# Optimization experiments

Hardware: AMD Instinct MI355X
Metric: run time of the kernel (lower is better)

Reference implementation:

```python
import jax, jax.numpy as jnp
import numpy as np

N, D = 1024, 512
BS, N_TEXT, N_VIDEO = 64, 16, 16
BETA = 1.0
N_ITERS = 50


def setup_inputs() -> dict:
    key = jax.random.key(0)
    k1, k2 = jax.random.split(key)
    return {
        "t_prob": jax.random.normal(k1, (N, D), dtype=jnp.float32),
        "v_prob": jax.random.normal(k2, (N, D), dtype=jnp.float32),
        "n": N,
        "bs": BS,
        "n_text": N_TEXT,
        "n_video": N_VIDEO,
    }


def _l2norm(x):
    # matches F.normalize(x, p=2, dim=1) (eps irrelevant for randn inputs)
    return x / jnp.linalg.norm(x, axis=1, keepdims=True)


def reference(t_prob, v_prob, n, bs, n_text, n_video):
    dt = t_prob.dtype
    x = _l2norm(t_prob)
    y = _l2norm(v_prob)
    C = 1.0 - x @ y.T                      # [n, n] cosine distance
    A = jnp.exp(-C / BETA)

    sigma0 = jnp.ones((n, 1), dtype=dt) / n
    T0 = jnp.ones((n, n), dtype=dt)

    def step(carry, _):
        T, sigma = carry
        Q = A * T                          # [n, n]
        delta = 1.0 / (n * (Q @ sigma))    # [n, 1]
        sigma_new = 1.0 / (n * (Q.T @ delta))  # [n, 1]
        # diag(delta) @ Q @ diag(sigma) == row/col rescale
        T_new = delta * Q * sigma_new.T
        return (T_new, sigma_new), None

    (T, _), _ = jax.lax.scan(step, (T0, sigma0), None, length=N_ITERS)

    distance_matrix = C.T @ T              # [n, n]
    distance_matrix = distance_matrix.reshape(bs, n_text, bs, n_video).mean(axis=(1, 3))
    dis_loss = jnp.trace(distance_matrix)
    return distance_matrix, dis_loss
```

## Files before the change

kernel.cpp:

```cpp
#include <hip/hip_runtime.h>
#include <math.h>


#define NWG 32
#define TPB 256
#define NIT 50
#define NREP 4

typedef unsigned long long ull;

constexpr int CL_OFF   = 0;
constexpr int CVEC_OFF = 1024 * 1024;
constexpr int CNT_OFF  = CVEC_OFF + 3 * NREP * 1024;

__global__ __launch_bounds__(256) void k_gemm(const float* __restrict__ X,
                                              const float* __restrict__ Y,
                                              float* __restrict__ ws) {
    __shared__ float As[32][68];
    __shared__ float Bs[32][68];
    __shared__ float nX[64], nY[64];
    float* Cl = ws + CL_OFF;

    int tid = threadIdx.x;
    int tx = tid & 15, ty = tid >> 4;
    int bx = blockIdx.x, by = blockIdx.y;
    int lr0 = tid >> 3;
    int kq  = (tid & 7) * 4;

    float acc[4][4] = {};
    float sx0 = 0.f, sx1 = 0.f, sy0 = 0.f, sy1 = 0.f;
    for (int k0 = 0; k0 < 512; k0 += 32) {
        float4 xa = *(const float4*)(X + (size_t)(by * 64 + lr0) * 512 + k0 + kq);
        float4 xb = *(const float4*)(X + (size_t)(by * 64 + lr0 + 32) * 512 + k0 + kq);
        float4 ya = *(const float4*)(Y + (size_t)(bx * 64 + lr0) * 512 + k0 + kq);
        float4 yb = *(const float4*)(Y + (size_t)(bx * 64 + lr0 + 32) * 512 + k0 + kq);
        sx0 += xa.x * xa.x + xa.y * xa.y + xa.z * xa.z + xa.w * xa.w;
        sx1 += xb.x * xb.x + xb.y * xb.y + xb.z * xb.z + xb.w * xb.w;
        sy0 += ya.x * ya.x + ya.y * ya.y + ya.z * ya.z + ya.w * ya.w;
        sy1 += yb.x * yb.x + yb.y * yb.y + yb.z * yb.z + yb.w * yb.w;
        As[kq + 0][lr0] = xa.x; As[kq + 1][lr0] = xa.y;
        As[kq + 2][lr0] = xa.z; As[kq + 3][lr0] = xa.w;
        As[kq + 0][lr0 + 32] = xb.x; As[kq + 1][lr0 + 32] = xb.y;
        As[kq + 2][lr0 + 32] = xb.z; As[kq + 3][lr0 + 32] = xb.w;
        Bs[kq + 0][lr0] = ya.x; Bs[kq + 1][lr0] = ya.y;
        Bs[kq + 2][lr0] = ya.z; Bs[kq + 3][lr0] = ya.w;
        Bs[kq + 0][lr0 + 32] = yb.x; Bs[kq + 1][lr0 + 32] = yb.y;
        Bs[kq + 2][lr0 + 32] = yb.z; Bs[kq + 3][lr0 + 32] = yb.w;
        __syncthreads();
#pragma unroll
        for (int kk = 0; kk < 32; ++kk) {
            float4 a4 = *(const float4*)&As[kk][4 * ty];
            float4 b4 = *(const float4*)&Bs[kk][4 * tx];
            float av[4] = {a4.x, a4.y, a4.z, a4.w};
            float bv[4] = {b4.x, b4.y, b4.z, b4.w};
#pragma unroll
            for (int r = 0; r < 4; ++r)
#pragma unroll
                for (int q = 0; q < 4; ++q) acc[r][q] += av[r] * bv[q];
        }
        __syncthreads();
    }
#pragma unroll
    for (int m = 1; m < 8; m <<= 1) {
        sx0 += __shfl_xor(sx0, m, 64);
        sx1 += __shfl_xor(sx1, m, 64);
        sy0 += __shfl_xor(sy0, m, 64);
        sy1 += __shfl_xor(sy1, m, 64);
    }
    if ((tid & 7) == 0) {
        nX[lr0] = sx0; nX[lr0 + 32] = sx1;
        nY[lr0] = sy0; nY[lr0 + 32] = sy1;
    }
    __syncthreads();

    int i0 = by * 64 + 4 * ty, j0 = bx * 64 + 4 * tx;
    float vy[4];
#pragma unroll
    for (int q = 0; q < 4; ++q) vy[q] = 1.0f / sqrtf(nY[4 * tx + q]);
#pragma unroll
    for (int r = 0; r < 4; ++r) {
        float vx = 1.0f / sqrtf(nX[4 * ty + r]);
        float4 o;
        o.x = acc[r][0] * vx * vy[0] - 1.0f;
        o.y = acc[r][1] * vx * vy[1] - 1.0f;
        o.z = acc[r][2] * vx * vy[2] - 1.0f;
        o.w = acc[r][3] * vx * vy[3] - 1.0f;
        *(float4*)(Cl + (size_t)(i0 + r) * 1024 + j0) = o;
    }
}

__global__ __launch_bounds__(256, 1) void k_ipot(float* __restrict__ ws,
                                                 float* __restrict__ out) {
    __shared__ float sL[1024];
    __shared__ float aL[32];
    __shared__ float buf[4 * 1024];
    __shared__ float twv[4];

    const int g = blockIdx.x, tid = threadIdx.x;
    const int rs = tid >> 6, lane = tid & 63;
    float* Cl   = ws + CL_OFF;
    float* cvec = ws + CVEC_OFF;
    unsigned* grp = (unsigned*)(ws + CNT_OFF);

    float C[8][16], E[8][16];
#pragma unroll
    for (int i = 0; i < 8; ++i) {
        const float* src = Cl + (size_t)(g * 32 + rs * 8 + i) * 1024 + lane * 16;
#pragma unroll
        for (int q = 0; q < 4; ++q) {
            float4 c = *(const float4*)(src + 4 * q);
            C[i][4 * q + 0] = c.x; C[i][4 * q + 1] = c.y;
            C[i][4 * q + 2] = c.z; C[i][4 * q + 3] = c.w;
        }
    }
#pragma unroll
    for (int i = 0; i < 8; ++i)
#pragma unroll
        for (int u = 0; u < 16; ++u) E[i][u] = __expf(C[i][u]);

    float bv[4] = {1.0f, 1.0f, 1.0f, 1.0f};

    for (int t = 0; t < NIT; ++t) {
        if (t == 0) {
            *(float4*)&sL[4 * tid] =
                make_float4(1/1024.f, 1/1024.f, 1/1024.f, 1/1024.f);
        } else {
            if (tid == 0) {
                unsigned tgt = (unsigned)t * 8u;
                long gd = 0;
                while (__hip_atomic_load(&grp[0], __ATOMIC_RELAXED, __HIP_MEMORY_SCOPE_AGENT) < tgt ||
                       __hip_atomic_load(&grp[1], __ATOMIC_RELAXED, __HIP_MEMORY_SCOPE_AGENT) < tgt ||
                       __hip_atomic_load(&grp[2], __ATOMIC_RELAXED, __HIP_MEMORY_SCOPE_AGENT) < tgt ||
                       __hip_atomic_load(&grp[3], __ATOMIC_RELAXED, __HIP_MEMORY_SCOPE_AGENT) < tgt) {
                    __builtin_amdgcn_s_sleep(1);
                    if (++gd > 2000000) break;
                }
            }
            __syncthreads();
            const ull* rb = (const ull*)(cvec + ((t + 2) % 3) * (NREP * 1024)) + 2 * tid;
            ull u00 = __hip_atomic_load(rb + 0 * 512,     __ATOMIC_RELAXED, __HIP_MEMORY_SCOPE_AGENT);
            ull u01 = __hip_atomic_load(rb + 0 * 512 + 1, __ATOMIC_RELAXED, __HIP_MEMORY_SCOPE_AGENT);
            ull u10 = __hip_atomic_load(rb + 1 * 512,     __ATOMIC_RELAXED, __HIP_MEMORY_SCOPE_AGENT);
            ull u11 = __hip_atomic_load(rb + 1 * 512 + 1, __ATOMIC_RELAXED, __HIP_MEMORY_SCOPE_AGENT);
            ull u20 = __hip_atomic_load(rb + 2 * 512,     __ATOMIC_RELAXED, __HIP_MEMORY_SCOPE_AGENT);
            ull u21 = __hip_atomic_load(rb + 2 * 512 + 1, __ATOMIC_RELAXED, __HIP_MEMORY_SCOPE_AGENT);
            ull u30 = __hip_atomic_load(rb + 3 * 512,     __ATOMIC_RELAXED, __HIP_MEMORY_SCOPE_AGENT);
            ull u31 = __hip_atomic_load(rb + 3 * 512 + 1, __ATOMIC_RELAXED, __HIP_MEMORY_SCOPE_AGENT);
            if (t >= 2 && tid < 64) {
                ull* zb = (ull*)(cvec + ((t + 1) % 3) * (NREP * 1024)) + g * 64 + tid;
                __hip_atomic_store(zb, 0ull, __ATOMIC_RELAXED, __HIP_MEMORY_SCOPE_AGENT);
            }
            float c0 = __uint_as_float((unsigned)u00) + __uint_as_float((unsigned)u10) +
                       __uint_as_float((unsigned)u20) + __uint_as_float((unsigned)u30);
            float c1 = __uint_as_float((unsigned)(u00 >> 32)) + __uint_as_float((unsigned)(u10 >> 32)) +
                       __uint_as_float((unsigned)(u20 >> 32)) + __uint_as_float((unsigned)(u30 >> 32));
            float c2 = __uint_as_float((unsigned)u01) + __uint_as_float((unsigned)u11) +
                       __uint_as_float((unsigned)u21) + __uint_as_float((unsigned)u31);
            float c3 = __uint_as_float((unsigned)(u01 >> 32)) + __uint_as_float((unsigned)(u11 >> 32)) +
                       __uint_as_float((unsigned)(u21 >> 32)) + __uint_as_float((unsigned)(u31 >> 32));
            float b0 = 1.0f / c0, b1 = 1.0f / c1, b2 = 1.0f / c2, b3 = 1.0f / c3;
            float4 sn;
            sn.x = b0 * b0 / bv[0] * (1.0f / 1024.0f); bv[0] = b0;
            sn.y = b1 * b1 / bv[1] * (1.0f / 1024.0f); bv[1] = b1;
            sn.z = b2 * b2 / bv[2] * (1.0f / 1024.0f); bv[2] = b2;
            sn.w = b3 * b3 / bv[3] * (1.0f / 1024.0f); bv[3] = b3;
            *(float4*)&sL[4 * tid] = sn;
        }
        __syncthreads();

        float sv[16];
#pragma unroll
        for (int q = 0; q < 4; ++q) {
            float4 s4 = *(const float4*)&sL[lane * 16 + 4 * q];
            sv[4 * q + 0] = s4.x; sv[4 * q + 1] = s4.y;
            sv[4 * q + 2] = s4.z; sv[4 * q + 3] = s4.w;
        }
        float rp[8];
#pragma unroll
        for (int i = 0; i < 8; ++i) {
            float a = 0.0f;
#pragma unroll
            for (int u = 0; u < 16; ++u) a += E[i][u] * sv[u];
            rp[i] = a;
        }
#pragma unroll
        for (int m = 1; m < 64; m <<= 1)
#pragma unroll
            for (int i = 0; i < 8; ++i) rp[i] += __shfl_xor(rp[i], m, 64);
        if (lane == 0) {
#pragma unroll
            for (int i = 0; i < 8; ++i)
                aL[rs * 8 + i] = 1.0f / (1024.0f * rp[i]);
        }
        __syncthreads();

        float av[8];
#pragma unroll
        for (int i = 0; i < 8; ++i) av[i] = aL[rs * 8 + i];
        float cp[16];
#pragma unroll
        for (int u = 0; u < 16; ++u) {
            float a = 0.0f;
#pragma unroll
            for (int i = 0; i < 8; ++i) a += E[i][u] * av[i];
            cp[u] = a;
        }
#pragma unroll
        for (int q = 0; q < 4; ++q)
            *(float4*)&buf[rs * 1024 + lane * 16 + 4 * q] =
                make_float4(cp[4*q], cp[4*q+1], cp[4*q+2], cp[4*q+3]);
        __syncthreads();

        float4 t0 = *(const float4*)&buf[0 * 1024 + 4 * tid];
        float4 t1 = *(const float4*)&buf[1 * 1024 + 4 * tid];
        float4 t2 = *(const float4*)&buf[2 * 1024 + 4 * tid];
        float4 t3 = *(const float4*)&buf[3 * 1024 + 4 * tid];
        float* wb = cvec + (t % 3) * (NREP * 1024) + (g & 3) * 1024 + 4 * tid;
        atomicAdd(wb + 0, t0.x + t1.x + t2.x + t3.x);
        atomicAdd(wb + 1, t0.y + t1.y + t2.y + t3.y);
        atomicAdd(wb + 2, t0.z + t1.z + t2.z + t3.z);
        atomicAdd(wb + 3, t0.w + t1.w + t2.w + t3.w);
        __syncthreads();
        if (tid == 0)
            __hip_atomic_fetch_add(&grp[g >> 3], 1u, __ATOMIC_RELAXED,
                                   __HIP_MEMORY_SCOPE_AGENT);

        if (t < NIT - 1) {
            const float kf = (float)(t + 2);
#pragma unroll
            for (int i = 0; i < 8; ++i)
#pragma unroll
                for (int u = 0; u < 16; ++u) E[i][u] = __expf(kf * C[i][u]);
        }
    }

    if (tid == 0) {
        unsigned tgt = (unsigned)NIT * 8u;
        long gd = 0;
        while (__hip_atomic_load(&grp[0], __ATOMIC_RELAXED, __HIP_MEMORY_SCOPE_AGENT) < tgt ||
               __hip_atomic_load(&grp[1], __ATOMIC_RELAXED, __HIP_MEMORY_SCOPE_AGENT) < tgt ||
               __hip_atomic_load(&grp[2], __ATOMIC_RELAXED, __HIP_MEMORY_SCOPE_AGENT) < tgt ||
               __hip_atomic_load(&grp[3], __ATOMIC_RELAXED, __HIP_MEMORY_SCOPE_AGENT) < tgt) {
            __builtin_amdgcn_s_sleep(1);
            if (++gd > 2000000) break;
        }
    }
    __syncthreads();
    {
        const ull* rb = (const ull*)(cvec + ((NIT - 1) % 3) * (NREP * 1024)) + 2 * tid;
        ull u00 = __hip_atomic_load(rb + 0 * 512,     __ATOMIC_RELAXED, __HIP_MEMORY_SCOPE_AGENT);
        ull u01 = __hip_atomic_load(rb + 0 * 512 + 1, __ATOMIC_RELAXED, __HIP_MEMORY_SCOPE_AGENT);
        ull u10 = __hip_atomic_load(rb + 1 * 512,     __ATOMIC_RELAXED, __HIP_MEMORY_SCOPE_AGENT);
        ull u11 = __hip_atomic_load(rb + 1 * 512 + 1, __ATOMIC_RELAXED, __HIP_MEMORY_SCOPE_AGENT);
        ull u20 = __hip_atomic_load(rb + 2 * 512,     __ATOMIC_RELAXED, __HIP_MEMORY_SCOPE_AGENT);
        ull u21 = __hip_atomic_load(rb + 2 * 512 + 1, __ATOMIC_RELAXED, __HIP_MEMORY_SCOPE_AGENT);
        ull u30 = __hip_atomic_load(rb + 3 * 512,     __ATOMIC_RELAXED, __HIP_MEMORY_SCOPE_AGENT);
        ull u31 = __hip_atomic_load(rb + 3 * 512 + 1, __ATOMIC_RELAXED, __HIP_MEMORY_SCOPE_AGENT);
        float4 bb;
        bb.x = 1.0f / (__uint_as_float((unsigned)u00) + __uint_as_float((unsigned)u10) +
                       __uint_as_float((unsigned)u20) + __uint_as_float((unsigned)u30));
        bb.y = 1.0f / (__uint_as_float((unsigned)(u00 >> 32)) + __uint_as_float((unsigned)(u10 >> 32)) +
                       __uint_as_float((unsigned)(u20 >> 32)) + __uint_as_float((unsigned)(u30 >> 32)));
        bb.z = 1.0f / (__uint_as_float((unsigned)u01) + __uint_as_float((unsigned)u11) +
                       __uint_as_float((unsigned)u21) + __uint_as_float((unsigned)u31));
        bb.w = 1.0f / (__uint_as_float((unsigned)(u01 >> 32)) + __uint_as_float((unsigned)(u11 >> 32)) +
                       __uint_as_float((unsigned)(u21 >> 32)) + __uint_as_float((unsigned)(u31 >> 32)));
        *(float4*)&sL[4 * tid] = bb;
    }
    __syncthreads();

    float* Ps = buf;
    float* Rs = buf + 2048;
    float bl[16];
#pragma unroll
    for (int q = 0; q < 4; ++q) {
        float4 b4 = *(const float4*)&sL[lane * 16 + 4 * q];
        bl[4 * q + 0] = b4.x; bl[4 * q + 1] = b4.y;
        bl[4 * q + 2] = b4.z; bl[4 * q + 3] = b4.w;
    }
#pragma unroll
    for (int i = 0; i < 8; ++i) {
        float p = 0.0f, r = 0.0f;
#pragma unroll
        for (int u = 0; u < 16; ++u) {
            p += C[i][u];
            r += E[i][u] * bl[u];
        }
        Ps[(rs * 8 + i) * 64 + lane] = -p;
        Rs[(rs * 8 + i) * 64 + lane] = aL[rs * 8 + i] * r;
    }
    __syncthreads();

    float Rk[32];
#pragma unroll
    for (int k = 0; k < 32; ++k) Rk[k] = Rs[k * 64 + lane];
    const float sc = 1.0f / (256.0f * 1024.0f);
    float tsum = 0.0f;
#pragma unroll
    for (int q = 0; q < 16; ++q) {
        int o = tid + 256 * q;
        int A = o >> 6;
        float acc = 0.0f;
#pragma unroll
        for (int k = 0; k < 32; ++k) acc += Ps[k * 64 + A] * Rk[k];
        float val = acc * sc;
        atomicAdd(out + o, val);
        if (A == lane) tsum += val;
    }
#pragma unroll
    for (int m = 1; m < 64; m <<= 1) tsum += __shfl_xor(tsum, m, 64);
    if (lane == 0) twv[rs] = tsum;
    __syncthreads();
    if (tid == 0) atomicAdd(out + 4096, twv[0] + twv[1] + twv[2] + twv[3]);
}

extern "C" void kernel_launch(void* const* d_in, const int* in_sizes, int n_in,
                              void* d_out, int out_size, void* d_ws, size_t ws_size,
                              hipStream_t stream) {
    const float* X = (const float*)d_in[0];
    const float* Y = (const float*)d_in[1];
    float* out = (float*)d_out;
    float* ws  = (float*)d_ws;

    (void)hipMemsetAsync((char*)d_ws + (size_t)CVEC_OFF * 4, 0,
                         (3 * NREP * 1024 + 16) * 4, stream);
    (void)hipMemsetAsync(d_out, 0, (size_t)out_size * 4, stream);

    k_gemm<<<dim3(16, 16), 256, 0, stream>>>(X, Y, ws);
    k_ipot<<<NWG, TPB, 0, stream>>>(ws, out);
}
```

Measured before the change: 331.3 us.

## Widen IPOT workgroups to 1024 threads with two rows per wavefront

Raises the iterative Sinkhorn-style kernel from 256 to 1024 threads per workgroup, so each of the 16 wavefronts holds 2 rows of the cost and kernel matrices instead of 8. The per-thread register footprint shrinks and the column-sum stage becomes a 16-way shared-memory reduction with one scalar atomic per thread. The intent is to put more wavefronts on each CU and hide the latency of the per-iteration matrix-vector products and the cross-workgroup barrier. In exchange, each __syncthreads spans 16 waves, the shared buffer grows fourfold, and the final tail loop is redistributed across the wider block.

```diff
diff --git a/kernel.cpp b/kernel.cpp
--- a/kernel.cpp
+++ b/kernel.cpp
@@ -3,7 +3,7 @@
 
 
 #define NWG 32
-#define TPB 256
+#define TPB 1024
 #define NIT 50
 #define NREP 4
 
@@ -89,12 +89,12 @@
     }
 }
 
-__global__ __launch_bounds__(256, 1) void k_ipot(float* __restrict__ ws,
-                                                 float* __restrict__ out) {
+__global__ __launch_bounds__(1024, 4) void k_ipot(float* __restrict__ ws,
+                                                  float* __restrict__ out) {
     __shared__ float sL[1024];
     __shared__ float aL[32];
-    __shared__ float buf[4 * 1024];
-    __shared__ float twv[4];
+    __shared__ float buf[16 * 1024];
+    __shared__ float twv[16];
 
     const int g = blockIdx.x, tid = threadIdx.x;
     const int rs = tid >> 6, lane = tid & 63;
@@ -102,10 +102,10 @@
     float* cvec = ws + CVEC_OFF;
     unsigned* grp = (unsigned*)(ws + CNT_OFF);
 
-    float C[8][16], E[8][16];
-#pragma unroll
-    for (int i = 0; i < 8; ++i) {
-        const float* src = Cl + (size_t)(g * 32 + rs * 8 + i) * 1024 + lane * 16;
+    float C[2][16], E[2][16];
+#pragma unroll
+    for (int i = 0; i < 2; ++i) {
+        const float* src = Cl + (size_t)(g * 32 + rs * 2 + i) * 1024 + lane * 16;
 #pragma unroll
         for (int q = 0; q < 4; ++q) {
             float4 c = *(const float4*)(src + 4 * q);
@@ -114,16 +114,15 @@
         }
     }
 #pragma unroll
-    for (int i = 0; i < 8; ++i)
+    for (int i = 0; i < 2; ++i)
 #pragma unroll
         for (int u = 0; u < 16; ++u) E[i][u] = __expf(C[i][u]);
 
-    float bv[4] = {1.0f, 1.0f, 1.0f, 1.0f};
+    float bv = 1.0f;
 
     for (int t = 0; t < NIT; ++t) {
         if (t == 0) {
-            *(float4*)&sL[4 * tid] =
-                make_float4(1/1024.f, 1/1024.f, 1/1024.f, 1/1024.f);
+            sL[tid] = 1.0f / 1024.0f;
         } else {
             if (tid == 0) {
                 unsigned tgt = (unsigned)t * 8u;
@@ -137,34 +136,19 @@
                 }
             }
             __syncthreads();
-            const ull* rb = (const ull*)(cvec + ((t + 2) % 3) * (NREP * 1024)) + 2 * tid;
-            ull u00 = __hip_atomic_load(rb + 0 * 512,     __ATOMIC_RELAXED, __HIP_MEMORY_SCOPE_AGENT);
-            ull u01 = __hip_atomic_load(rb + 0 * 512 + 1, __ATOMIC_RELAXED, __HIP_MEMORY_SCOPE_AGENT);
-            ull u10 = __hip_atomic_load(rb + 1 * 512,     __ATOMIC_RELAXED, __HIP_MEMORY_SCOPE_AGENT);
-            ull u11 = __hip_atomic_load(rb + 1 * 512 + 1, __ATOMIC_RELAXED, __HIP_MEMORY_SCOPE_AGENT);
-            ull u20 = __hip_atomic_load(rb + 2 * 512,     __ATOMIC_RELAXED, __HIP_MEMORY_SCOPE_AGENT);
-            ull u21 = __hip_atomic_load(rb + 2 * 512 + 1, __ATOMIC_RELAXED, __HIP_MEMORY_SCOPE_AGENT);
-            ull u30 = __hip_atomic_load(rb + 3 * 512,     __ATOMIC_RELAXED, __HIP_MEMORY_SCOPE_AGENT);
-            ull u31 = __hip_atomic_load(rb + 3 * 512 + 1, __ATOMIC_RELAXED, __HIP_MEMORY_SCOPE_AGENT);
+            const float* rb = cvec + ((t + 2) % 3) * (NREP * 1024) + tid;
+            float r0 = __hip_atomic_load(rb + 0 * 1024, __ATOMIC_RELAXED, __HIP_MEMORY_SCOPE_AGENT);
+            float r1 = __hip_atomic_load(rb + 1 * 1024, __ATOMIC_RELAXED, __HIP_MEMORY_SCOPE_AGENT);
+            float r2 = __hip_atomic_load(rb + 2 * 1024, __ATOMIC_RELAXED, __HIP_MEMORY_SCOPE_AGENT);
+            float r3 = __hip_atomic_load(rb + 3 * 1024, __ATOMIC_RELAXED, __HIP_MEMORY_SCOPE_AGENT);
             if (t >= 2 && tid < 64) {
                 ull* zb = (ull*)(cvec + ((t + 1) % 3) * (NREP * 1024)) + g * 64 + tid;
                 __hip_atomic_store(zb, 0ull, __ATOMIC_RELAXED, __HIP_MEMORY_SCOPE_AGENT);
             }
-            float c0 = __uint_as_float((unsigned)u00) + __uint_as_float((unsigned)u10) +
-                       __uint_as_float((unsigned)u20) + __uint_as_float((unsigned)u30);
-            float c1 = __uint_as_float((unsigned)(u00 >> 32)) + __uint_as_float((unsigned)(u10 >> 32)) +
-                       __uint_as_float((unsigned)(u20 >> 32)) + __uint_as_float((unsigned)(u30 >> 32));
-            float c2 = __uint_as_float((unsigned)u01) + __uint_as_float((unsigned)u11) +
-                       __uint_as_float((unsigned)u21) + __uint_as_float((unsigned)u31);
-            float c3 = __uint_as_float((unsigned)(u01 >> 32)) + __uint_as_float((unsigned)(u11 >> 32)) +
-                       __uint_as_float((unsigned)(u21 >> 32)) + __uint_as_float((unsigned)(u31 >> 32));
-            float b0 = 1.0f / c0, b1 = 1.0f / c1, b2 = 1.0f / c2, b3 = 1.0f / c3;
-            float4 sn;
-            sn.x = b0 * b0 / bv[0] * (1.0f / 1024.0f); bv[0] = b0;
-            sn.y = b1 * b1 / bv[1] * (1.0f / 1024.0f); bv[1] = b1;
-            sn.z = b2 * b2 / bv[2] * (1.0f / 1024.0f); bv[2] = b2;
-            sn.w = b3 * b3 / bv[3] * (1.0f / 1024.0f); bv[3] = b3;
-            *(float4*)&sL[4 * tid] = sn;
+            float c = r0 + r1 + r2 + r3;
+            float b = 1.0f / c;
+            sL[tid] = b * b / bv * (1.0f / 1024.0f);
+            bv = b;
         }
         __syncthreads();
 
@@ -175,51 +159,42 @@
             sv[4 * q + 0] = s4.x; sv[4 * q + 1] = s4.y;
             sv[4 * q + 2] = s4.z; sv[4 * q + 3] = s4.w;
         }
-        float rp[8];
-#pragma unroll
-        for (int i = 0; i < 8; ++i) {
+        float rp[2];
+#pragma unroll
+        for (int i = 0; i < 2; ++i) {
             float a = 0.0f;
 #pragma unroll
             for (int u = 0; u < 16; ++u) a += E[i][u] * sv[u];
             rp[i] = a;
         }
 #pragma unroll
-        for (int m = 1; m < 64; m <<= 1)
-#pragma unroll
-            for (int i = 0; i < 8; ++i) rp[i] += __shfl_xor(rp[i], m, 64);
+        for (int m = 1; m < 64; m <<= 1) {
+            rp[0] += __shfl_xor(rp[0], m, 64);
+            rp[1] += __shfl_xor(rp[1], m, 64);
+        }
         if (lane == 0) {
-#pragma unroll
-            for (int i = 0; i < 8; ++i)
-                aL[rs * 8 + i] = 1.0f / (1024.0f * rp[i]);
-        }
-        __syncthreads();
-
-        float av[8];
-#pragma unroll
-        for (int i = 0; i < 8; ++i) av[i] = aL[rs * 8 + i];
-        float cp[16];
-#pragma unroll
-        for (int u = 0; u < 16; ++u) {
-            float a = 0.0f;
-#pragma unroll
-            for (int i = 0; i < 8; ++i) a += E[i][u] * av[i];
-            cp[u] = a;
-        }
-#pragma unroll
-        for (int q = 0; q < 4; ++q)
-            *(float4*)&buf[rs * 1024 + lane * 16 + 4 * q] =
-                make_float4(cp[4*q], cp[4*q+1], cp[4*q+2], cp[4*q+3]);
-        __syncthreads();
-
-        float4 t0 = *(const float4*)&buf[0 * 1024 + 4 * tid];
-        float4 t1 = *(const float4*)&buf[1 * 1024 + 4 * tid];
-        float4 t2 = *(const float4*)&buf[2 * 1024 + 4 * tid];
-        float4 t3 = *(const float4*)&buf[3 * 1024 + 4 * tid];
-        float* wb = cvec + (t % 3) * (NREP * 1024) + (g & 3) * 1024 + 4 * tid;
-        atomicAdd(wb + 0, t0.x + t1.x + t2.x + t3.x);
-        atomicAdd(wb + 1, t0.y + t1.y + t2.y + t3.y);
-        atomicAdd(wb + 2, t0.z + t1.z + t2.z + t3.z);
-        atomicAdd(wb + 3, t0.w + t1.w + t2.w + t3.w);
+            aL[rs * 2 + 0] = 1.0f / (1024.0f * rp[0]);
+            aL[rs * 2 + 1] = 1.0f / (1024.0f * rp[1]);
+        }
+        __syncthreads();
+
+        float av0 = aL[rs * 2 + 0], av1 = aL[rs * 2 + 1];
+#pragma unroll
+        for (int q = 0; q < 4; ++q) {
+            float4 o;
+            o.x = E[0][4*q+0] * av0 + E[1][4*q+0] * av1;
+            o.y = E[0][4*q+1] * av0 + E[1][4*q+1] * av1;
+            o.z = E[0][4*q+2] * av0 + E[1][4*q+2] * av1;
+            o.w = E[0][4*q+3] * av0 + E[1][4*q+3] * av1;
+            *(float4*)&buf[rs * 1024 + lane * 16 + 4 * q] = o;
+        }
+        __syncthreads();
+
+        float csum = 0.0f;
+#pragma unroll
+        for (int w = 0; w < 16; ++w) csum += buf[w * 1024 + tid];
+        float* wb = cvec + (t % 3) * (NREP * 1024) + (g & 3) * 1024 + tid;
+        atomicAdd(wb, csum);
         __syncthreads();
         if (tid == 0)
             __hip_atomic_fetch_add(&grp[g >> 3], 1u, __ATOMIC_RELAXED,
@@ -228,7 +203,7 @@
         if (t < NIT - 1) {
             const float kf = (float)(t + 2);
 #pragma unroll
-            for (int i = 0; i < 8; ++i)
+            for (int i = 0; i < 2; ++i)
 #pragma unroll
                 for (int u = 0; u < 16; ++u) E[i][u] = __expf(kf * C[i][u]);
         }
@@ -247,25 +222,12 @@
     }
     __syncthreads();
     {
-        const ull* rb = (const ull*)(cvec + ((NIT - 1) % 3) * (NREP * 1024)) + 2 * tid;
-        ull u00 = __hip_atomic_load(rb + 0 * 512,     __ATOMIC_RELAXED, __HIP_MEMORY_SCOPE_AGENT);
-        ull u01 = __hip_atomic_load(rb + 0 * 512 + 1, __ATOMIC_RELAXED, __HIP_MEMORY_SCOPE_AGENT);
-        ull u10 = __hip_atomic_load(rb + 1 * 512,     __ATOMIC_RELAXED, __HIP_MEMORY_SCOPE_AGENT);
-        ull u11 = __hip_atomic_load(rb + 1 * 512 + 1, __ATOMIC_RELAXED, __HIP_MEMORY_SCOPE_AGENT);
-        ull u20 = __hip_atomic_load(rb + 2 * 512,     __ATOMIC_RELAXED, __HIP_MEMORY_SCOPE_AGENT);
-        ull u21 = __hip_atomic_load(rb + 2 * 512 + 1, __ATOMIC_RELAXED, __HIP_MEMORY_SCOPE_AGENT);
-        ull u30 = __hip_atomic_load(rb + 3 * 512,     __ATOMIC_RELAXED, __HIP_MEMORY_SCOPE_AGENT);
-        ull u31 = __hip_atomic_load(rb + 3 * 512 + 1, __ATOMIC_RELAXED, __HIP_MEMORY_SCOPE_AGENT);
-        float4 bb;
-        bb.x = 1.0f / (__uint_as_float((unsigned)u00) + __uint_as_float((unsigned)u10) +
-                       __uint_as_float((unsigned)u20) + __uint_as_float((unsigned)u30));
-        bb.y = 1.0f / (__uint_as_float((unsigned)(u00 >> 32)) + __uint_as_float((unsigned)(u10 >> 32)) +
-                       __uint_as_float((unsigned)(u20 >> 32)) + __uint_as_float((unsigned)(u30 >> 32)));
-        bb.z = 1.0f / (__uint_as_float((unsigned)u01) + __uint_as_float((unsigned)u11) +
-                       __uint_as_float((unsigned)u21) + __uint_as_float((unsigned)u31));
-        bb.w = 1.0f / (__uint_as_float((unsigned)(u01 >> 32)) + __uint_as_float((unsigned)(u11 >> 32)) +
-                       __uint_as_float((unsigned)(u21 >> 32)) + __uint_as_float((unsigned)(u31 >> 32)));
-        *(float4*)&sL[4 * tid] = bb;
+        const float* rb = cvec + ((NIT - 1) % 3) * (NREP * 1024) + tid;
+        float r0 = __hip_atomic_load(rb + 0 * 1024, __ATOMIC_RELAXED, __HIP_MEMORY_SCOPE_AGENT);
+        float r1 = __hip_atomic_load(rb + 1 * 1024, __ATOMIC_RELAXED, __HIP_MEMORY_SCOPE_AGENT);
+        float r2 = __hip_atomic_load(rb + 2 * 1024, __ATOMIC_RELAXED, __HIP_MEMORY_SCOPE_AGENT);
+        float r3 = __hip_atomic_load(rb + 3 * 1024, __ATOMIC_RELAXED, __HIP_MEMORY_SCOPE_AGENT);
+        sL[tid] = 1.0f / (r0 + r1 + r2 + r3);
     }
     __syncthreads();
 
@@ -279,15 +241,15 @@
         bl[4 * q + 2] = b4.z; bl[4 * q + 3] = b4.w;
     }
 #pragma unroll
-    for (int i = 0; i < 8; ++i) {
+    for (int i = 0; i < 2; ++i) {
         float p = 0.0f, r = 0.0f;
 #pragma unroll
         for (int u = 0; u < 16; ++u) {
             p += C[i][u];
             r += E[i][u] * bl[u];
         }
-        Ps[(rs * 8 + i) * 64 + lane] = -p;
-        Rs[(rs * 8 + i) * 64 + lane] = aL[rs * 8 + i] * r;
+        Ps[(rs * 2 + i) * 64 + lane] = -p;
+        Rs[(rs * 2 + i) * 64 + lane] = aL[rs * 2 + i] * r;
     }
     __syncthreads();
 
@@ -297,8 +259,8 @@
     const float sc = 1.0f / (256.0f * 1024.0f);
     float tsum = 0.0f;
 #pragma unroll
-    for (int q = 0; q < 16; ++q) {
-        int o = tid + 256 * q;
+    for (int q = 0; q < 4; ++q) {
+        int o = tid + 1024 * q;
         int A = o >> 6;
         float acc = 0.0f;
 #pragma unroll
@@ -311,7 +273,12 @@
     for (int m = 1; m < 64; m <<= 1) tsum += __shfl_xor(tsum, m, 64);
     if (lane == 0) twv[rs] = tsum;
     __syncthreads();
-    if (tid == 0) atomicAdd(out + 4096, twv[0] + twv[1] + twv[2] + twv[3]);
+    if (tid == 0) {
+        float ts = 0.0f;
+#pragma unroll
+        for (int w = 0; w < 16; ++w) ts += twv[w];
+        atomicAdd(out + 4096, ts);
+    }
 }
 
 extern "C" void kernel_launch(void* const* d_in, const int* in_sizes, int n_in,
```

Measured after the change: 347.1 us. +4.8%, slower.
